# Performance work log

Hardware: AMD Instinct MI355X
Metric: run time of the kernel (lower is better)

The kernel has to match this reference:

```python
import jax, jax.numpy as jnp
import numpy as np

N = 40000
K = 16
NUM_CLASSES = 8
BN_EPS = 1e-5


def _mlp(h, W1, b1, g, bt, m, v, W2, b2):
    # Linear -> ReLU -> BatchNorm1d (eval mode, running stats) -> Linear
    h = jax.nn.relu(h @ W1 + b1)
    h = (h - m) / jnp.sqrt(v + BN_EPS) * g + bt
    return h @ W2 + b2


def _normals(pos, nbr):
    # cross product of first two neighbor offsets, normalized; fallback [0,0,1]
    v1 = pos[nbr[:, 0]] - pos
    v2 = pos[nbr[:, 1]] - pos
    n = jnp.cross(v1, v2)
    nrm = jnp.linalg.norm(n, axis=-1, keepdims=True)
    unit = n / jnp.maximum(nrm, 1e-12)
    up = jnp.array([0.0, 0.0, 1.0], dtype=pos.dtype)
    return jnp.where(nrm > 0, unit, up)


def _pointnet_conv(x, pos, nbr_all, W1, b1, g, bt, m, v, W2, b2):
    # PyG PointNetConv: msg = local_nn(cat[x_j, pos_j - pos_i]); max-aggregate
    xj = x[nbr_all]                        # [N, K+1, F]
    rel = pos[nbr_all] - pos[:, None, :]   # [N, K+1, 3]
    msg = _mlp(jnp.concatenate([xj, rel], axis=-1), W1, b1, g, bt, m, v, W2, b2)
    return msg.max(axis=1)


def setup_inputs():
    key = jax.random.key(0)
    ks = jax.random.split(key, 32)

    def lin_w(k, fi, fo):
        return (jax.random.normal(k, (fi, fo), jnp.float32) / np.sqrt(fi)).astype(jnp.float32)

    def vec(k, d, scale=0.01):
        return scale * jax.random.normal(k, (d,), jnp.float32)

    return {
        "pos": jax.random.normal(ks[0], (N, 3), jnp.float32),
        "neighbor_idx": jax.random.randint(ks[1], (N, K), 0, N),
        # local_features: Linear(9,64), ReLU, BN(64), Linear(64,128)
        "W1": lin_w(ks[2], 9, 64), "b1": vec(ks[3], 64),
        "g1": 1.0 + 0.1 * jax.random.normal(ks[4], (64,), jnp.float32),
        "bt1": vec(ks[5], 64), "m1": vec(ks[6], 64, 0.1),
        "v1": jax.random.uniform(ks[7], (64,), jnp.float32, minval=0.5, maxval=1.5),
        "W2": lin_w(ks[8], 64, 128), "b2": vec(ks[9], 128),
        # roof_features: Linear(131,128), ReLU, BN(128), Linear(128,256)
        "W3": lin_w(ks[10], 131, 128), "b3": vec(ks[11], 128),
        "g2": 1.0 + 0.1 * jax.random.normal(ks[12], (128,), jnp.float32),
        "bt2": vec(ks[13], 128), "m2": vec(ks[14], 128, 0.1),
        "v2": jax.random.uniform(ks[15], (128,), jnp.float32, minval=0.5, maxval=1.5),
        "W4": lin_w(ks[16], 128, 256), "b4": vec(ks[17], 256),
        # classifier: Linear(256, num_classes)
        "Wc": lin_w(ks[18], 256, NUM_CLASSES), "bc": vec(ks[19], NUM_CLASSES),
    }


def reference(pos, neighbor_idx, W1, b1, g1, bt1, m1, v1, W2, b2,
              W3, b3, g2, bt2, m2, v2, W4, b4, Wc, bc):
    x = pos  # data.x is used as both features and coordinates
    normals = _normals(pos, neighbor_idx)
    x = jnp.concatenate([x, normals], axis=1)  # [N, 6]
    # PointNetConv adds self-loops by default
    self_idx = jnp.arange(pos.shape[0], dtype=neighbor_idx.dtype)[:, None]
    nbr_all = jnp.concatenate([neighbor_idx, self_idx], axis=1)  # [N, K+1]
    x = jax.nn.relu(_pointnet_conv(x, pos, nbr_all, W1, b1, g1, bt1, m1, v1, W2, b2))
    x = jax.nn.relu(_pointnet_conv(x, pos, nbr_all, W3, b3, g2, bt2, m2, v2, W4, b4))
    logits = x @ Wc + bc
    return jax.nn.log_softmax(logits, axis=-1)
```

## Files before the change

kernel.cpp:

```cpp
#include <hip/hip_runtime.h>
#include <math.h>

#define NPTS 40000
#define KNBR 16
#define BN_EPS 1e-5f

typedef __attribute__((ext_vector_type(8))) short v8s;
typedef __attribute__((ext_vector_type(4))) float f32x4;

__device__ __forceinline__ unsigned short f2bf(float f) {
    union { float f; unsigned int u; } c; c.f = f;
    unsigned int u = c.u + 0x7fffu + ((c.u >> 16) & 1u);
    return (unsigned short)(u >> 16);
}
__device__ __forceinline__ float bflo(unsigned int u) {
    union { unsigned int u; float f; } c; c.u = u << 16; return c.f;
}
__device__ __forceinline__ float bfhi(unsigned int u) {
    union { unsigned int u; float f; } c; c.u = u & 0xffff0000u; return c.f;
}

__global__ __launch_bounds__(256, 4)
void k1_b1(const float* __restrict__ pos, const int* __restrict__ nbr,
           const float* __restrict__ W1, const float* __restrict__ b1,
           unsigned short* __restrict__ B1) {
    int p = blockIdx.x * 4 + (threadIdx.x >> 6);
    int k = threadIdx.x & 63;
    float px = pos[p * 3 + 0], py = pos[p * 3 + 1], pz = pos[p * 3 + 2];
    int n0 = nbr[p * KNBR + 0], n1 = nbr[p * KNBR + 1];
    float ax = pos[n0 * 3 + 0] - px, ay = pos[n0 * 3 + 1] - py, az = pos[n0 * 3 + 2] - pz;
    float bx = pos[n1 * 3 + 0] - px, by = pos[n1 * 3 + 1] - py, bz = pos[n1 * 3 + 2] - pz;
    float cx = ay * bz - az * by;
    float cy = az * bx - ax * bz;
    float cz = ax * by - ay * bx;
    float nrm = sqrtf(cx * cx + cy * cy + cz * cz);
    float inv = 1.0f / fmaxf(nrm, 1e-12f);
    float ux, uy, uz;
    if (nrm > 0.0f) { ux = cx * inv; uy = cy * inv; uz = cz * inv; }
    else            { ux = 0.0f;     uy = 0.0f;     uz = 1.0f;     }
    float acc = b1[k];
    acc = fmaf(px, W1[0 * 64 + k], acc);
    acc = fmaf(py, W1[1 * 64 + k], acc);
    acc = fmaf(pz, W1[2 * 64 + k], acc);
    acc = fmaf(ux, W1[3 * 64 + k], acc);
    acc = fmaf(uy, W1[4 * 64 + k], acc);
    acc = fmaf(uz, W1[5 * 64 + k], acc);
    B1[p * 64 + k] = f2bf(acc);
}

#define PTS2 32
__global__ __launch_bounds__(256, 2)
void k2_conv1_mfma(const float* __restrict__ pos, const int* __restrict__ nbr,
                   const unsigned short* __restrict__ B1, const float* __restrict__ W1,
                   const float* __restrict__ g1, const float* __restrict__ bt1,
                   const float* __restrict__ m1, const float* __restrict__ v1,
                   const float* __restrict__ W2, const float* __restrict__ b2,
                   const float* __restrict__ W3, const float* __restrict__ b3,
                   unsigned short* __restrict__ A2) {
    __shared__ __align__(16) unsigned char Tl[2][16 * 128];
    __shared__ __align__(16) unsigned char Hl[32 * 256];
    __shared__ float Ssf1[32 * 128];

    const int tid  = threadIdx.x;
    const int wv   = tid >> 6;
    const int lane = tid & 63;
    const int lgrp = lane >> 4;
    const int lmod = lane & 15;

    v8s Bf2[2][2];
    float b2c[2];
#pragma unroll
    for (int nt = 0; nt < 2; ++nt) {
        const int col = wv * 32 + nt * 16 + lmod;
        b2c[nt] = b2[col];
#pragma unroll
        for (int kt = 0; kt < 2; ++kt)
#pragma unroll
            for (int j = 0; j < 8; ++j)
                Bf2[nt][kt][j] = (short)f2bf(W2[(kt * 32 + lgrp * 8 + j) * 128 + col]);
    }
    const int ch0 = (lane & 31) * 2;
    const int rsub = lane >> 5;
    const float w6a = W1[6 * 64 + ch0],     w7a = W1[7 * 64 + ch0],     w8a = W1[8 * 64 + ch0];
    const float w6b = W1[6 * 64 + ch0 + 1], w7b = W1[7 * 64 + ch0 + 1], w8b = W1[8 * 64 + ch0 + 1];
    const float s1a = g1[ch0] * rsqrtf(v1[ch0] + BN_EPS);
    const float o1a = bt1[ch0] - m1[ch0] * s1a;
    const float s1b = g1[ch0 + 1] * rsqrtf(v1[ch0 + 1] + BN_EPS);
    const float o1b = bt1[ch0 + 1] - m1[ch0 + 1] * s1b;

    const int base = blockIdx.x * PTS2;

#pragma unroll
    for (int pr = 0; pr < 16; ++pr) {
        const int pl = pr * 2 + rsub;
        const unsigned int a = *(const unsigned int*)&B1[(size_t)(base + pl) * 64 + ch0];
        const float ta = fmaf(fmaxf(bflo(a), 0.f), s1a, o1a);
        const float tb = fmaf(fmaxf(bfhi(a), 0.f), s1b, o1b);
        const unsigned int w = (unsigned int)f2bf(ta) | ((unsigned int)f2bf(tb) << 16);
        const int row = pl & 15;
        int byte = row * 128 + ch0 * 2;
        byte ^= (row & 7) << 4;
        *(unsigned int*)(Tl[pl >> 4] + byte) = w;
    }
    __syncthreads();
    {
        f32x4 accS[2][2];
#pragma unroll
        for (int hf = 0; hf < 2; ++hf)
#pragma unroll
            for (int nt = 0; nt < 2; ++nt) accS[hf][nt] = f32x4{0.f, 0.f, 0.f, 0.f};
#pragma unroll
        for (int hf = 0; hf < 2; ++hf)
#pragma unroll
            for (int kt = 0; kt < 2; ++kt) {
                int b0 = lmod * 128 + kt * 64 + lgrp * 16;
                b0 ^= (lmod & 7) << 4;
                const v8s a0 = *(const v8s*)(Tl[hf] + b0);
#pragma unroll
                for (int nt = 0; nt < 2; ++nt)
                    accS[hf][nt] = __builtin_amdgcn_mfma_f32_16x16x32_bf16(a0, Bf2[nt][kt], accS[hf][nt], 0, 0, 0);
            }
#pragma unroll
        for (int hf = 0; hf < 2; ++hf)
#pragma unroll
            for (int nt = 0; nt < 2; ++nt)
#pragma unroll
                for (int reg = 0; reg < 4; ++reg)
                    Ssf1[(hf * 16 + lgrp * 4 + reg) * 128 + wv * 32 + nt * 16 + lmod] = accS[hf][nt][reg];
    }
    __syncthreads();

    {
        const int i = base;
        const float cx = pos[i * 3 + 0], cy = pos[i * 3 + 1], cz = pos[i * 3 + 2];
#pragma unroll
        for (int it = 0; it < 2; ++it) {
            const int m = it * 8 + wv * 2 + rsub;
            const int idx = nbr[i * KNBR + m];
            const unsigned int a = *(const unsigned int*)&B1[(size_t)idx * 64 + ch0];
            const float rx = pos[idx * 3 + 0] - cx;
            const float ry = pos[idx * 3 + 1] - cy;
            const float rz = pos[idx * 3 + 2] - cz;
            float pa = bflo(a);
            pa = fmaf(rx, w6a, pa); pa = fmaf(ry, w7a, pa); pa = fmaf(rz, w8a, pa);
            float pb = bfhi(a);
            pb = fmaf(rx, w6b, pb); pb = fmaf(ry, w7b, pb); pb = fmaf(rz, w8b, pb);
            const float ta = fmaf(fmaxf(pa, 0.f), s1a, o1a);
            const float tb = fmaf(fmaxf(pb, 0.f), s1b, o1b);
            const unsigned int w = (unsigned int)f2bf(ta) | ((unsigned int)f2bf(tb) << 16);
            int byte = m * 128 + ch0 * 2;
            byte ^= (m & 7) << 4;
            *(unsigned int*)(Tl[0] + byte) = w;
        }
    }
    unsigned int aCur[2], aNxt[2];
    float pCx[2], pCy[2], pCz[2], pNx[2], pNy[2], pNz[2];
#pragma unroll
    for (int it = 0; it < 2; ++it) { aCur[it] = 0u; aNxt[it] = 0u; pCx[it]=pCy[it]=pCz[it]=pNx[it]=pNy[it]=pNz[it]=0.f; }
    {
        const int in_ = base + 1;
#pragma unroll
        for (int it = 0; it < 2; ++it) {
            const int m = it * 8 + wv * 2 + rsub;
            const int idx = nbr[in_ * KNBR + m];
            aCur[it] = *(const unsigned int*)&B1[(size_t)idx * 64 + ch0];
            pCx[it] = pos[idx * 3 + 0]; pCy[it] = pos[idx * 3 + 1]; pCz[it] = pos[idx * 3 + 2];
        }
    }
    __syncthreads();

    for (int p = 0; p < PTS2; ++p) {
        const int buf = p & 1;
        if (p < PTS2 - 2) {
            const int in2 = base + p + 2;
#pragma unroll
            for (int it = 0; it < 2; ++it) {
                const int m = it * 8 + wv * 2 + rsub;
                const int idx = nbr[in2 * KNBR + m];
                aNxt[it] = *(const unsigned int*)&B1[(size_t)idx * 64 + ch0];
                pNx[it] = pos[idx * 3 + 0]; pNy[it] = pos[idx * 3 + 1]; pNz[it] = pos[idx * 3 + 2];
            }
        }
        f32x4 acc0[2];
        acc0[0] = f32x4{0.f, 0.f, 0.f, 0.f};
        acc0[1] = f32x4{0.f, 0.f, 0.f, 0.f};
#pragma unroll
        for (int kt = 0; kt < 2; ++kt) {
            int b0 = lmod * 128 + kt * 64 + lgrp * 16;
            b0 ^= (lmod & 7) << 4;
            const v8s a0 = *(const v8s*)(Tl[buf] + b0);
#pragma unroll
            for (int nt = 0; nt < 2; ++nt)
                acc0[nt] = __builtin_amdgcn_mfma_f32_16x16x32_bf16(a0, Bf2[nt][kt], acc0[nt], 0, 0, 0);
        }
#pragma unroll
        for (int nt = 0; nt < 2; ++nt) {
            float mv = fmaxf(fmaxf(acc0[nt][0], acc0[nt][1]),
                             fmaxf(acc0[nt][2], acc0[nt][3]));
            mv = fmaxf(mv, __shfl_xor(mv, 16));
            mv = fmaxf(mv, __shfl_xor(mv, 32));
            const float ss = Ssf1[p * 128 + wv * 32 + nt * 16 + lmod];
            const float h = fmaxf(fmaxf(mv, ss) + b2c[nt], 0.f);
            if (lgrp == 0) {
                int hb = p * 256 + (wv * 32 + nt * 16 + lmod) * 2;
                hb ^= (p & 7) << 4;
                *(unsigned short*)(Hl + hb) = f2bf(h);
            }
        }
        if (p < PTS2 - 1) {
            const int in_ = base + p + 1;
            const float ccx = pos[in_ * 3 + 0], ccy = pos[in_ * 3 + 1], ccz = pos[in_ * 3 + 2];
#pragma unroll
            for (int it = 0; it < 2; ++it) {
                const int m = it * 8 + wv * 2 + rsub;
                const float rx = pCx[it] - ccx, ry = pCy[it] - ccy, rz = pCz[it] - ccz;
                float pa = bflo(aCur[it]);
                pa = fmaf(rx, w6a, pa); pa = fmaf(ry, w7a, pa); pa = fmaf(rz, w8a, pa);
                float pb = bfhi(aCur[it]);
                pb = fmaf(rx, w6b, pb); pb = fmaf(ry, w7b, pb); pb = fmaf(rz, w8b, pb);
                const float ta = fmaf(fmaxf(pa, 0.f), s1a, o1a);
                const float tb = fmaf(fmaxf(pb, 0.f), s1b, o1b);
                const unsigned int w = (unsigned int)f2bf(ta) | ((unsigned int)f2bf(tb) << 16);
                int byte = m * 128 + ch0 * 2;
                byte ^= (m & 7) << 4;
                *(unsigned int*)(Tl[buf ^ 1] + byte) = w;
            }
        }
        __syncthreads();
#pragma unroll
        for (int it = 0; it < 2; ++it) {
            aCur[it] = aNxt[it];
            pCx[it] = pNx[it]; pCy[it] = pNy[it]; pCz[it] = pNz[it];
        }
    }

    v8s Wf3[2][4];
    float b3c[2];
#pragma unroll
    for (int nt = 0; nt < 2; ++nt) {
        const int col = wv * 32 + nt * 16 + lmod;
        b3c[nt] = b3[col];
#pragma unroll
        for (int kt = 0; kt < 4; ++kt)
#pragma unroll
            for (int j = 0; j < 8; ++j)
                Wf3[nt][kt][j] = (short)f2bf(W3[(kt * 32 + lgrp * 8 + j) * 128 + col]);
    }
    f32x4 accA[2][2];
#pragma unroll
    for (int mt = 0; mt < 2; ++mt)
#pragma unroll
        for (int nt = 0; nt < 2; ++nt) accA[mt][nt] = f32x4{0.f, 0.f, 0.f, 0.f};
#pragma unroll
    for (int kt = 0; kt < 4; ++kt) {
#pragma unroll
        for (int mt = 0; mt < 2; ++mt) {
            int ba = (mt * 16 + lmod) * 256 + kt * 64 + lgrp * 16;
            ba ^= (lmod & 7) << 4;
            const v8s aH = *(const v8s*)(Hl + ba);
#pragma unroll
            for (int nt = 0; nt < 2; ++nt)
                accA[mt][nt] = __builtin_amdgcn_mfma_f32_16x16x32_bf16(aH, Wf3[nt][kt], accA[mt][nt], 0, 0, 0);
        }
    }
#pragma unroll
    for (int mt = 0; mt < 2; ++mt)
#pragma unroll
        for (int nt = 0; nt < 2; ++nt)
#pragma unroll
            for (int reg = 0; reg < 4; ++reg) {
                const int row = base + mt * 16 + lgrp * 4 + reg;
                const int col = wv * 32 + nt * 16 + lmod;
                A2[(size_t)row * 128 + col] = f2bf(accA[mt][nt][reg] + b3c[nt]);
            }
}

#define PTS4 32
__global__ __launch_bounds__(256, 2)
void k4_conv2_mfma(const float* __restrict__ pos, const int* __restrict__ nbr,
                   const unsigned short* __restrict__ A2, const float* __restrict__ W3,
                   const float* __restrict__ g2, const float* __restrict__ bt2,
                   const float* __restrict__ m2, const float* __restrict__ v2,
                   const float* __restrict__ W4, const float* __restrict__ b4,
                   const float* __restrict__ Wc,
                   float* __restrict__ Z) {
    __shared__ __align__(16) unsigned char Tl[2][16 * 256];
    __shared__ float Ssf[32 * 256];

    const int tid  = threadIdx.x;
    const int wv   = tid >> 6;
    const int lane = tid & 63;
    const int lgrp = lane >> 4;
    const int lmod = lane & 15;

    v8s Bf[4][4];
#pragma unroll
    for (int nt = 0; nt < 4; ++nt) {
        const int col = wv * 64 + nt * 16 + lmod;
#pragma unroll
        for (int kt = 0; kt < 4; ++kt)
#pragma unroll
            for (int j = 0; j < 8; ++j)
                Bf[nt][kt][j] = (short)f2bf(W4[(kt * 32 + lgrp * 8 + j) * 256 + col]);
    }
    float wcls[4][8]; float b4c[4];
#pragma unroll
    for (int nt = 0; nt < 4; ++nt) {
        const int col = wv * 64 + nt * 16 + lmod;
        b4c[nt] = b4[col];
#pragma unroll
        for (int c = 0; c < 8; ++c) wcls[nt][c] = Wc[col * 8 + c];
    }
    const int ch0 = lane * 2;
    const float bw0a = W3[128 * 128 + ch0],     bw1a = W3[129 * 128 + ch0],     bw2a = W3[130 * 128 + ch0];
    const float bw0b = W3[128 * 128 + ch0 + 1], bw1b = W3[129 * 128 + ch0 + 1], bw2b = W3[130 * 128 + ch0 + 1];
    const float sa = g2[ch0] * rsqrtf(v2[ch0] + BN_EPS);
    const float oa = bt2[ch0] - m2[ch0] * sa;
    const float sb = g2[ch0 + 1] * rsqrtf(v2[ch0 + 1] + BN_EPS);
    const float ob = bt2[ch0 + 1] - m2[ch0 + 1] * sb;

    const int base = blockIdx.x * PTS4;

#pragma unroll
    for (int pl = 0; pl < 16; ++pl) {
        {
            const unsigned int a = *(const unsigned int*)&A2[(size_t)(base + pl) * 128 + ch0];
            const float ta = fmaf(fmaxf(bflo(a), 0.f), sa, oa);
            const float tb = fmaf(fmaxf(bfhi(a), 0.f), sb, ob);
            const unsigned int w = (unsigned int)f2bf(ta) | ((unsigned int)f2bf(tb) << 16);
            int byte = pl * 256 + ch0 * 2;
            byte ^= (pl & 7) << 4;
            *(unsigned int*)(Tl[0] + byte) = w;
        }
        {
            const unsigned int a = *(const unsigned int*)&A2[(size_t)(base + 16 + pl) * 128 + ch0];
            const float ta = fmaf(fmaxf(bflo(a), 0.f), sa, oa);
            const float tb = fmaf(fmaxf(bfhi(a), 0.f), sb, ob);
            const unsigned int w = (unsigned int)f2bf(ta) | ((unsigned int)f2bf(tb) << 16);
            int byte = pl * 256 + ch0 * 2;
            byte ^= (pl & 7) << 4;
            *(unsigned int*)(Tl[1] + byte) = w;
        }
    }
    __syncthreads();
    {
        f32x4 accS[2][4];
#pragma unroll
        for (int hf = 0; hf < 2; ++hf)
#pragma unroll
            for (int nt = 0; nt < 4; ++nt) accS[hf][nt] = f32x4{0.f, 0.f, 0.f, 0.f};
#pragma unroll
        for (int hf = 0; hf < 2; ++hf)
#pragma unroll
            for (int kt = 0; kt < 4; ++kt) {
                int b0 = lmod * 256 + kt * 64 + lgrp * 16;
                b0 ^= (lmod & 7) << 4;
                const v8s a0 = *(const v8s*)(Tl[hf] + b0);
#pragma unroll
                for (int nt = 0; nt < 4; ++nt)
                    accS[hf][nt] = __builtin_amdgcn_mfma_f32_16x16x32_bf16(a0, Bf[nt][kt], accS[hf][nt], 0, 0, 0);
            }
#pragma unroll
        for (int hf = 0; hf < 2; ++hf)
#pragma unroll
            for (int nt = 0; nt < 4; ++nt)
#pragma unroll
                for (int reg = 0; reg < 4; ++reg)
                    Ssf[(hf * 16 + lgrp * 4 + reg) * 256 + wv * 64 + nt * 16 + lmod] = accS[hf][nt][reg];
    }
    __syncthreads();

    {
        const int i = base;
        const float cx = pos[i * 3 + 0], cy = pos[i * 3 + 1], cz = pos[i * 3 + 2];
#pragma unroll
        for (int it = 0; it < 4; ++it) {
            const int m = it * 4 + wv;
            const int idx = nbr[i * KNBR + m];
            const unsigned int a = *(const unsigned int*)&A2[(size_t)idx * 128 + ch0];
            const float rx = pos[idx * 3 + 0] - cx;
            const float ry = pos[idx * 3 + 1] - cy;
            const float rz = pos[idx * 3 + 2] - cz;
            float pa = bflo(a);
            pa = fmaf(rx, bw0a, pa); pa = fmaf(ry, bw1a, pa); pa = fmaf(rz, bw2a, pa);
            float pb = bfhi(a);
            pb = fmaf(rx, bw0b, pb); pb = fmaf(ry, bw1b, pb); pb = fmaf(rz, bw2b, pb);
            const float ta = fmaf(fmaxf(pa, 0.f), sa, oa);
            const float tb = fmaf(fmaxf(pb, 0.f), sb, ob);
            const unsigned int w = (unsigned int)f2bf(ta) | ((unsigned int)f2bf(tb) << 16);
            int byte = m * 256 + ch0 * 2;
            byte ^= (m & 7) << 4;
            *(unsigned int*)(Tl[0] + byte) = w;
        }
    }
    unsigned int aCur[4], aNxt[4];
    float pCx[4], pCy[4], pCz[4], pNx[4], pNy[4], pNz[4];
#pragma unroll
    for (int it = 0; it < 4; ++it) { aCur[it] = 0u; aNxt[it] = 0u; pCx[it]=pCy[it]=pCz[it]=pNx[it]=pNy[it]=pNz[it]=0.f; }
    {
        const int in_ = base + 1;
#pragma unroll
        for (int it = 0; it < 4; ++it) {
            const int m = it * 4 + wv;
            const int idx = nbr[in_ * KNBR + m];
            aCur[it] = *(const unsigned int*)&A2[(size_t)idx * 128 + ch0];
            pCx[it] = pos[idx * 3 + 0]; pCy[it] = pos[idx * 3 + 1]; pCz[it] = pos[idx * 3 + 2];
        }
    }
    __syncthreads();

    for (int p = 0; p < PTS4; ++p) {
        const int buf = p & 1;
        if (p < PTS4 - 2) {
            const int in2 = base + p + 2;
#pragma unroll
            for (int it = 0; it < 4; ++it) {
                const int m = it * 4 + wv;
                const int idx = nbr[in2 * KNBR + m];
                aNxt[it] = *(const unsigned int*)&A2[(size_t)idx * 128 + ch0];
                pNx[it] = pos[idx * 3 + 0]; pNy[it] = pos[idx * 3 + 1]; pNz[it] = pos[idx * 3 + 2];
            }
        }
        f32x4 acc0[4];
#pragma unroll
        for (int nt = 0; nt < 4; ++nt) acc0[nt] = f32x4{0.f, 0.f, 0.f, 0.f};
#pragma unroll
        for (int kt = 0; kt < 4; ++kt) {
            int b0 = lmod * 256 + kt * 64 + lgrp * 16;
            b0 ^= (lmod & 7) << 4;
            const v8s a0 = *(const v8s*)(Tl[buf] + b0);
#pragma unroll
            for (int nt = 0; nt < 4; ++nt)
                acc0[nt] = __builtin_amdgcn_mfma_f32_16x16x32_bf16(a0, Bf[nt][kt], acc0[nt], 0, 0, 0);
        }
        float part[8];
#pragma unroll
        for (int c = 0; c < 8; ++c) part[c] = 0.f;
#pragma unroll
        for (int nt = 0; nt < 4; ++nt) {
            float mv = fmaxf(fmaxf(acc0[nt][0], acc0[nt][1]),
                             fmaxf(acc0[nt][2], acc0[nt][3]));
            mv = fmaxf(mv, __shfl_xor(mv, 16));
            mv = fmaxf(mv, __shfl_xor(mv, 32));
            const float ss = Ssf[p * 256 + wv * 64 + nt * 16 + lmod];
            const float h = fmaxf(fmaxf(mv, ss) + b4c[nt], 0.f);
#pragma unroll
            for (int c = 0; c < 8; ++c) part[c] = fmaf(h, wcls[nt][c], part[c]);
        }
#pragma unroll
        for (int c = 0; c < 8; ++c) {
            part[c] += __shfl_xor(part[c], 1);
            part[c] += __shfl_xor(part[c], 2);
            part[c] += __shfl_xor(part[c], 4);
            part[c] += __shfl_xor(part[c], 8);
        }
        if (lane == 0) {
#pragma unroll
            for (int c = 0; c < 8; ++c)
                Z[(size_t)(base + p) * 32 + wv * 8 + c] = part[c];
        }
        if (p < PTS4 - 1) {
            const int in_ = base + p + 1;
            const float ccx = pos[in_ * 3 + 0], ccy = pos[in_ * 3 + 1], ccz = pos[in_ * 3 + 2];
#pragma unroll
            for (int it = 0; it < 4; ++it) {
                const int m = it * 4 + wv;
                const float rx = pCx[it] - ccx, ry = pCy[it] - ccy, rz = pCz[it] - ccz;
                float pa = bflo(aCur[it]);
                pa = fmaf(rx, bw0a, pa); pa = fmaf(ry, bw1a, pa); pa = fmaf(rz, bw2a, pa);
                float pb = bfhi(aCur[it]);
                pb = fmaf(rx, bw0b, pb); pb = fmaf(ry, bw1b, pb); pb = fmaf(rz, bw2b, pb);
                const float ta = fmaf(fmaxf(pa, 0.f), sa, oa);
                const float tb = fmaf(fmaxf(pb, 0.f), sb, ob);
                const unsigned int w = (unsigned int)f2bf(ta) | ((unsigned int)f2bf(tb) << 16);
                int byte = m * 256 + ch0 * 2;
                byte ^= (m & 7) << 4;
                *(unsigned int*)(Tl[buf ^ 1] + byte) = w;
            }
        }
        __syncthreads();
#pragma unroll
        for (int it = 0; it < 4; ++it) {
            aCur[it] = aNxt[it];
            pCx[it] = pNx[it]; pCy[it] = pNy[it]; pCz[it] = pNz[it];
        }
    }
}

__global__ __launch_bounds__(256, 4)
void k5_softmax(const float* __restrict__ Z, const float* __restrict__ bc,
                float* __restrict__ out) {
    const int i = blockIdx.x * 256 + threadIdx.x;
    if (i >= NPTS) return;
    float z[8];
#pragma unroll
    for (int c = 0; c < 8; ++c) z[c] = bc[c];
#pragma unroll
    for (int w = 0; w < 4; ++w) {
        const float4 a = *(const float4*)&Z[(size_t)i * 32 + w * 8 + 0];
        const float4 b = *(const float4*)&Z[(size_t)i * 32 + w * 8 + 4];
        z[0] += a.x; z[1] += a.y; z[2] += a.z; z[3] += a.w;
        z[4] += b.x; z[5] += b.y; z[6] += b.z; z[7] += b.w;
    }
    float mz = z[0];
#pragma unroll
    for (int c = 1; c < 8; ++c) mz = fmaxf(mz, z[c]);
    float se = 0.f;
#pragma unroll
    for (int c = 0; c < 8; ++c) se += expf(z[c] - mz);
    const float lse = mz + logf(se);
#pragma unroll
    for (int c = 0; c < 8; ++c) out[(size_t)i * 8 + c] = z[c] - lse;
}

extern "C" void kernel_launch(void* const* d_in, const int* in_sizes, int n_in,
                              void* d_out, int out_size, void* d_ws, size_t ws_size,
                              hipStream_t stream) {
    const float* pos = (const float*)d_in[0];
    const int*   nbr = (const int*)d_in[1];
    const float* W1  = (const float*)d_in[2];
    const float* b1  = (const float*)d_in[3];
    const float* g1  = (const float*)d_in[4];
    const float* bt1 = (const float*)d_in[5];
    const float* m1  = (const float*)d_in[6];
    const float* v1  = (const float*)d_in[7];
    const float* W2  = (const float*)d_in[8];
    const float* b2  = (const float*)d_in[9];
    const float* W3  = (const float*)d_in[10];
    const float* b3  = (const float*)d_in[11];
    const float* g2  = (const float*)d_in[12];
    const float* bt2 = (const float*)d_in[13];
    const float* m2  = (const float*)d_in[14];
    const float* v2  = (const float*)d_in[15];
    const float* W4  = (const float*)d_in[16];
    const float* b4  = (const float*)d_in[17];
    const float* Wc  = (const float*)d_in[18];
    const float* bc  = (const float*)d_in[19];
    float* out = (float*)d_out;

    unsigned short* B1 = (unsigned short*)d_ws;
    unsigned short* A2 = B1 + (size_t)NPTS * 64;
    float* Z = (float*)(A2 + (size_t)NPTS * 128);

    k1_b1<<<NPTS / 4, 256, 0, stream>>>(pos, nbr, W1, b1, B1);
    k2_conv1_mfma<<<NPTS / PTS2, 256, 0, stream>>>(pos, nbr, B1, W1, g1, bt1, m1, v1,
                                                   W2, b2, W3, b3, A2);
    k4_conv2_mfma<<<NPTS / PTS4, 256, 0, stream>>>(pos, nbr, A2, W3, g2, bt2, m2, v2,
                                                   W4, b4, Wc, Z);
    k5_softmax<<<(NPTS + 255) / 256, 256, 0, stream>>>(Z, bc, out);
}
```

Before: 320.9 us.

## Fuse classifier and log-softmax into conv2 kernel via MFMA; store self-term in bf16

The separate softmax kernel and the per-point classifier partial sums (eight shuffle reductions per point, written to a Z buffer) are removed. Conv2 now keeps the per-point hidden features in shared memory as bf16, and two waves compute the 256→8 classifier with MFMA before applying log-softmax in-register. The self-loop score buffers in both conv kernels switch from fp32 to bf16, halving their LDS footprint, which may raise occupancy but adds rounding. The staging loops are also redistributed across waves. This saves a launch and a global round trip, at the cost of extra LDS for H2 and idle waves during the final classifier step.

```diff
diff --git a/kernel.cpp b/kernel.cpp
--- a/kernel.cpp
+++ b/kernel.cpp
@@ -18,6 +18,9 @@
 }
 __device__ __forceinline__ float bfhi(unsigned int u) {
     union { unsigned int u; float f; } c; c.u = u & 0xffff0000u; return c.f;
+}
+__device__ __forceinline__ float bf2f(unsigned short u) {
+    union { unsigned int u; float f; } c; c.u = ((unsigned int)u) << 16; return c.f;
 }
 
 __global__ __launch_bounds__(256, 4)
@@ -59,7 +62,7 @@
                    unsigned short* __restrict__ A2) {
     __shared__ __align__(16) unsigned char Tl[2][16 * 128];
     __shared__ __align__(16) unsigned char Hl[32 * 256];
-    __shared__ float Ssf1[32 * 128];
+    __shared__ unsigned short Ssb[32 * 128];
 
     const int tid  = threadIdx.x;
     const int wv   = tid >> 6;
@@ -91,8 +94,8 @@
     const int base = blockIdx.x * PTS2;
 
 #pragma unroll
-    for (int pr = 0; pr < 16; ++pr) {
-        const int pl = pr * 2 + rsub;
+    for (int q = 0; q < 4; ++q) {
+        const int pl = wv * 8 + q * 2 + rsub;
         const unsigned int a = *(const unsigned int*)&B1[(size_t)(base + pl) * 64 + ch0];
         const float ta = fmaf(fmaxf(bflo(a), 0.f), s1a, o1a);
         const float tb = fmaf(fmaxf(bfhi(a), 0.f), s1b, o1b);
@@ -126,7 +129,8 @@
             for (int nt = 0; nt < 2; ++nt)
 #pragma unroll
                 for (int reg = 0; reg < 4; ++reg)
-                    Ssf1[(hf * 16 + lgrp * 4 + reg) * 128 + wv * 32 + nt * 16 + lmod] = accS[hf][nt][reg];
+                    Ssb[(hf * 16 + lgrp * 4 + reg) * 128 + wv * 32 + nt * 16 + lmod] =
+                        f2bf(accS[hf][nt][reg]);
     }
     __syncthreads();
 
@@ -199,7 +203,7 @@
                              fmaxf(acc0[nt][2], acc0[nt][3]));
             mv = fmaxf(mv, __shfl_xor(mv, 16));
             mv = fmaxf(mv, __shfl_xor(mv, 32));
-            const float ss = Ssf1[p * 128 + wv * 32 + nt * 16 + lmod];
+            const float ss = bf2f(Ssb[p * 128 + wv * 32 + nt * 16 + lmod]);
             const float h = fmaxf(fmaxf(mv, ss) + b2c[nt], 0.f);
             if (lgrp == 0) {
                 int hb = p * 256 + (wv * 32 + nt * 16 + lmod) * 2;
@@ -282,10 +286,11 @@
                    const float* __restrict__ g2, const float* __restrict__ bt2,
                    const float* __restrict__ m2, const float* __restrict__ v2,
                    const float* __restrict__ W4, const float* __restrict__ b4,
-                   const float* __restrict__ Wc,
-                   float* __restrict__ Z) {
+                   const float* __restrict__ Wc, const float* __restrict__ bc,
+                   float* __restrict__ out) {
     __shared__ __align__(16) unsigned char Tl[2][16 * 256];
-    __shared__ float Ssf[32 * 256];
+    __shared__ unsigned short Ssb[32 * 256];
+    __shared__ __align__(16) unsigned char H2[32 * 512];
 
     const int tid  = threadIdx.x;
     const int wv   = tid >> 6;
@@ -303,14 +308,9 @@
             for (int j = 0; j < 8; ++j)
                 Bf[nt][kt][j] = (short)f2bf(W4[(kt * 32 + lgrp * 8 + j) * 256 + col]);
     }
-    float wcls[4][8]; float b4c[4];
-#pragma unroll
-    for (int nt = 0; nt < 4; ++nt) {
-        const int col = wv * 64 + nt * 16 + lmod;
-        b4c[nt] = b4[col];
-#pragma unroll
-        for (int c = 0; c < 8; ++c) wcls[nt][c] = Wc[col * 8 + c];
-    }
+    float b4c[4];
+#pragma unroll
+    for (int nt = 0; nt < 4; ++nt) b4c[nt] = b4[wv * 64 + nt * 16 + lmod];
     const int ch0 = lane * 2;
     const float bw0a = W3[128 * 128 + ch0],     bw1a = W3[129 * 128 + ch0],     bw2a = W3[130 * 128 + ch0];
     const float bw0b = W3[128 * 128 + ch0 + 1], bw1b = W3[129 * 128 + ch0 + 1], bw2b = W3[130 * 128 + ch0 + 1];
@@ -322,25 +322,16 @@
     const int base = blockIdx.x * PTS4;
 
 #pragma unroll
-    for (int pl = 0; pl < 16; ++pl) {
-        {
-            const unsigned int a = *(const unsigned int*)&A2[(size_t)(base + pl) * 128 + ch0];
-            const float ta = fmaf(fmaxf(bflo(a), 0.f), sa, oa);
-            const float tb = fmaf(fmaxf(bfhi(a), 0.f), sb, ob);
-            const unsigned int w = (unsigned int)f2bf(ta) | ((unsigned int)f2bf(tb) << 16);
-            int byte = pl * 256 + ch0 * 2;
-            byte ^= (pl & 7) << 4;
-            *(unsigned int*)(Tl[0] + byte) = w;
-        }
-        {
-            const unsigned int a = *(const unsigned int*)&A2[(size_t)(base + 16 + pl) * 128 + ch0];
-            const float ta = fmaf(fmaxf(bflo(a), 0.f), sa, oa);
-            const float tb = fmaf(fmaxf(bfhi(a), 0.f), sb, ob);
-            const unsigned int w = (unsigned int)f2bf(ta) | ((unsigned int)f2bf(tb) << 16);
-            int byte = pl * 256 + ch0 * 2;
-            byte ^= (pl & 7) << 4;
-            *(unsigned int*)(Tl[1] + byte) = w;
-        }
+    for (int r = 0; r < 8; ++r) {
+        const int pl = wv * 8 + r;
+        const unsigned int a = *(const unsigned int*)&A2[(size_t)(base + pl) * 128 + ch0];
+        const float ta = fmaf(fmaxf(bflo(a), 0.f), sa, oa);
+        const float tb = fmaf(fmaxf(bfhi(a), 0.f), sb, ob);
+        const unsigned int w = (unsigned int)f2bf(ta) | ((unsigned int)f2bf(tb) << 16);
+        const int row = pl & 15;
+        int byte = row * 256 + ch0 * 2;
+        byte ^= (row & 7) << 4;
+        *(unsigned int*)(Tl[pl >> 4] + byte) = w;
     }
     __syncthreads();
     {
@@ -366,7 +357,8 @@
             for (int nt = 0; nt < 4; ++nt)
 #pragma unroll
                 for (int reg = 0; reg < 4; ++reg)
-                    Ssf[(hf * 16 + lgrp * 4 + reg) * 256 + wv * 64 + nt * 16 + lmod] = accS[hf][nt][reg];
+                    Ssb[(hf * 16 + lgrp * 4 + reg) * 256 + wv * 64 + nt * 16 + lmod] =
+                        f2bf(accS[hf][nt][reg]);
     }
     __syncthreads();
 
@@ -433,31 +425,19 @@
             for (int nt = 0; nt < 4; ++nt)
                 acc0[nt] = __builtin_amdgcn_mfma_f32_16x16x32_bf16(a0, Bf[nt][kt], acc0[nt], 0, 0, 0);
         }
-        float part[8];
-#pragma unroll
-        for (int c = 0; c < 8; ++c) part[c] = 0.f;
 #pragma unroll
         for (int nt = 0; nt < 4; ++nt) {
             float mv = fmaxf(fmaxf(acc0[nt][0], acc0[nt][1]),
                              fmaxf(acc0[nt][2], acc0[nt][3]));
             mv = fmaxf(mv, __shfl_xor(mv, 16));
             mv = fmaxf(mv, __shfl_xor(mv, 32));
-            const float ss = Ssf[p * 256 + wv * 64 + nt * 16 + lmod];
+            const float ss = bf2f(Ssb[p * 256 + wv * 64 + nt * 16 + lmod]);
             const float h = fmaxf(fmaxf(mv, ss) + b4c[nt], 0.f);
-#pragma unroll
-            for (int c = 0; c < 8; ++c) part[c] = fmaf(h, wcls[nt][c], part[c]);
-        }
-#pragma unroll
-        for (int c = 0; c < 8; ++c) {
-            part[c] += __shfl_xor(part[c], 1);
-            part[c] += __shfl_xor(part[c], 2);
-            part[c] += __shfl_xor(part[c], 4);
-            part[c] += __shfl_xor(part[c], 8);
-        }
-        if (lane == 0) {
-#pragma unroll
-            for (int c = 0; c < 8; ++c)
-                Z[(size_t)(base + p) * 32 + wv * 8 + c] = part[c];
+            if (lgrp == 0) {
+                int hb = p * 512 + (wv * 64 + nt * 16 + lmod) * 2;
+                hb ^= (p & 7) << 4;
+                *(unsigned short*)(H2 + hb) = f2bf(h);
+            }
         }
         if (p < PTS4 - 1) {
             const int in_ = base + p + 1;
@@ -485,32 +465,42 @@
             pCx[it] = pNx[it]; pCy[it] = pNy[it]; pCz[it] = pNz[it];
         }
     }
-}
-
-__global__ __launch_bounds__(256, 4)
-void k5_softmax(const float* __restrict__ Z, const float* __restrict__ bc,
-                float* __restrict__ out) {
-    const int i = blockIdx.x * 256 + threadIdx.x;
-    if (i >= NPTS) return;
-    float z[8];
-#pragma unroll
-    for (int c = 0; c < 8; ++c) z[c] = bc[c];
-#pragma unroll
-    for (int w = 0; w < 4; ++w) {
-        const float4 a = *(const float4*)&Z[(size_t)i * 32 + w * 8 + 0];
-        const float4 b = *(const float4*)&Z[(size_t)i * 32 + w * 8 + 4];
-        z[0] += a.x; z[1] += a.y; z[2] += a.z; z[3] += a.w;
-        z[4] += b.x; z[5] += b.y; z[6] += b.z; z[7] += b.w;
-    }
-    float mz = z[0];
-#pragma unroll
-    for (int c = 1; c < 8; ++c) mz = fmaxf(mz, z[c]);
-    float se = 0.f;
-#pragma unroll
-    for (int c = 0; c < 8; ++c) se += expf(z[c] - mz);
-    const float lse = mz + logf(se);
-#pragma unroll
-    for (int c = 0; c < 8; ++c) out[(size_t)i * 8 + c] = z[c] - lse;
+
+    if (wv < 2) {
+        v8s wcf[8];
+#pragma unroll
+        for (int kt = 0; kt < 8; ++kt)
+#pragma unroll
+            for (int j = 0; j < 8; ++j)
+                wcf[kt][j] = (lmod < 8)
+                    ? (short)f2bf(Wc[(kt * 32 + lgrp * 8 + j) * 8 + lmod])
+                    : (short)0;
+        f32x4 accZ = f32x4{0.f, 0.f, 0.f, 0.f};
+        const int row = wv * 16 + lmod;
+#pragma unroll
+        for (int kt = 0; kt < 8; ++kt) {
+            int ba = row * 512 + kt * 64 + lgrp * 16;
+            ba ^= (row & 7) << 4;
+            const v8s aH = *(const v8s*)(H2 + ba);
+            accZ = __builtin_amdgcn_mfma_f32_16x16x32_bf16(aH, wcf[kt], accZ, 0, 0, 0);
+        }
+        const float bcv = (lmod < 8) ? bc[lmod] : 0.f;
+#pragma unroll
+        for (int reg = 0; reg < 4; ++reg) {
+            const float z = accZ[reg] + bcv;
+            float mz = z;
+            mz = fmaxf(mz, __shfl_xor(mz, 1));
+            mz = fmaxf(mz, __shfl_xor(mz, 2));
+            mz = fmaxf(mz, __shfl_xor(mz, 4));
+            const float e = expf(z - mz);
+            float se = e;
+            se += __shfl_xor(se, 1);
+            se += __shfl_xor(se, 2);
+            se += __shfl_xor(se, 4);
+            if (lmod < 8)
+                out[(size_t)(base + wv * 16 + lgrp * 4 + reg) * 8 + lmod] = z - mz - logf(se);
+        }
+    }
 }
 
 extern "C" void kernel_launch(void* const* d_in, const int* in_sizes, int n_in,
@@ -540,12 +530,10 @@
 
     unsigned short* B1 = (unsigned short*)d_ws;
     unsigned short* A2 = B1 + (size_t)NPTS * 64;
-    float* Z = (float*)(A2 + (size_t)NPTS * 128);
 
     k1_b1<<<NPTS / 4, 256, 0, stream>>>(pos, nbr, W1, b1, B1);
     k2_conv1_mfma<<<NPTS / PTS2, 256, 0, stream>>>(pos, nbr, B1, W1, g1, bt1, m1, v1,
                                                    W2, b2, W3, b3, A2);
     k4_conv2_mfma<<<NPTS / PTS4, 256, 0, stream>>>(pos, nbr, A2, W3, g2, bt2, m2, v2,
-                                                   W4, b4, Wc, Z);
-    k5_softmax<<<(NPTS + 255) / 256, 256, 0, stream>>>(Z, bc, out);
-}
+                                                   W4, b4, Wc, bc, out);
+}
```

New measurement: 322.6 us. About the same (+0.5%).
